# Kernel optimization log

Measured on AMD Instinct MI355X. Metric: run time of the kernel, lower is better.

The kernel has to match this reference:

```python
import jax, jax.numpy as jnp
import numpy as np

N_QUBITS = 12
N_LAYERS = 3
N_PARAMS = N_QUBITS * 3 * N_LAYERS  # 108
BATCH = 8192
DIM = 1 << N_QUBITS  # 4096


def _rx(theta):
    c = jnp.cos(theta / 2).astype(jnp.complex64)
    s = jnp.sin(theta / 2).astype(jnp.complex64)
    return jnp.stack([jnp.stack([c, -1j * s]), jnp.stack([-1j * s, c])])


def _ry(theta):
    c = jnp.cos(theta / 2).astype(jnp.complex64)
    s = jnp.sin(theta / 2).astype(jnp.complex64)
    return jnp.stack([jnp.stack([c, -s]), jnp.stack([s, c])])


def _rz(theta):
    e = jnp.exp(-1j * theta.astype(jnp.complex64) / 2)
    z = jnp.zeros((), jnp.complex64)
    return jnp.stack([jnp.stack([e, z]), jnp.stack([z, jnp.conj(e)])])


def _apply_1q(state, q, U):
    # state: (B,) + (2,)*n ; apply 2x2 gate U on wire q (axis q+1)
    s = jnp.moveaxis(state, q + 1, -1)
    s = s @ U.T
    return jnp.moveaxis(s, -1, q + 1)


def _cnot(state, c, t):
    # control wire c, target wire t (axes offset by 1 for batch dim)
    ca, ta = c + 1, t + 1
    s0 = jax.lax.index_in_dim(state, 0, ca, keepdims=False)
    s1 = jax.lax.index_in_dim(state, 1, ca, keepdims=False)
    ta2 = ta - 1 if ta > ca else ta  # target axis shifts after removing control axis
    s1 = jnp.flip(s1, axis=ta2)  # X on target (size-2 axis)
    return jnp.stack([s0, s1], axis=ca)


def setup_inputs() -> dict:
    key = jax.random.key(0)
    k1, k2 = jax.random.split(key)
    x = jax.random.normal(k1, (BATCH, DIM), dtype=jnp.float32)
    params = jax.random.normal(k2, (N_PARAMS,), dtype=jnp.float32) * 0.1
    return {"x": x, "params": params}


def reference(x, params):
    n = N_QUBITS
    B = x.shape[0]
    # AmplitudeEmbedding with normalize=True
    norm = jnp.linalg.norm(x, axis=1, keepdims=True)
    state = (x / norm).astype(jnp.complex64).reshape((B,) + (2,) * n)
    idx = 0
    for _ in range(N_LAYERS):
        for q in range(n):
            state = _apply_1q(state, q, _rx(params[idx])); idx += 1
            state = _apply_1q(state, q, _ry(params[idx])); idx += 1
            state = _apply_1q(state, q, _rz(params[idx])); idx += 1
        for q in range(n):
            state = _cnot(state, q, (q + 1) % n)
    # <Z_q> = P(q=0) - P(q=1)
    p = state.real ** 2 + state.imag ** 2  # (B,) + (2,)*n, float32
    outs = []
    for q in range(n):
        axes = tuple(a for a in range(1, n + 1) if a != q + 1)
        marg = jnp.sum(p, axis=axes)  # (B, 2)
        outs.append(marg[:, 0] - marg[:, 1])
    return jnp.stack(outs, axis=1)  # (B, n_qubits)
```

## Files before the change

kernel.cpp:

```cpp
#include <hip/hip_runtime.h>
#include <math.h>

#define NQ 12
#define DIM 4096
#define NGATES 36
#define NROUND 9

typedef float f32x2 __attribute__((ext_vector_type(2)));

constexpr unsigned swz(unsigned x) { return x ^ (x >> 4); }

struct Round {
  unsigned s[4];
  unsigned l[4];
  unsigned cbsw8[16];
};
struct PlanT {
  Round rd[NROUND];
  unsigned zsel[NQ];
};

constexpr PlanT make_plan() {
  PlanT P{};
  unsigned Mcol[NQ] = {}, Minv[NQ] = {};
  for (int i = 0; i < NQ; ++i) { Mcol[i] = 1u << i; Minv[i] = 1u << i; }
  unsigned gm[NGATES] = {}, gs[NGATES] = {};
  int g = 0;
  for (int L = 0; L < 3; ++L) {
    for (int q = 0; q < NQ; ++q) { int b = NQ - 1 - q; gm[g] = Mcol[b]; gs[g] = Minv[b]; ++g; }
    for (int q = 0; q < NQ; ++q) {
      int bc = NQ - 1 - q, bt = NQ - 1 - ((q + 1) % NQ);
      Mcol[bc] ^= Mcol[bt];
      Minv[bt] ^= Minv[bc];
    }
  }
  for (int r = 0; r < NROUND; ++r) {
    unsigned m[4], red[4];
    for (int k = 0; k < 4; ++k) { m[k] = gm[4*r+k]; red[k] = m[k]; P.rd[r].s[k] = gs[4*r+k]; }
    for (int a = 0; a < 4; ++a) {
      unsigned p = red[a] & (0u - red[a]);
      for (int b = a + 1; b < 4; ++b) if (red[b] & p) red[b] ^= red[a];
    }
    unsigned piv[4];
    for (int a = 0; a < 4; ++a) piv[a] = red[a] & (0u - red[a]);
    for (int a = 0; a < 4; ++a)
      for (int b = a + 1; b < 4; ++b)
        if (piv[a] > piv[b]) { unsigned tp = piv[a]; piv[a] = piv[b]; piv[b] = tp; }
    for (int a = 0; a < 4; ++a) P.rd[r].l[a] = piv[a] - 1u;
    for (int d = 0; d < 16; ++d) {
      unsigned c = 0;
      for (int k = 0; k < 4; ++k) if (d & (1 << k)) c ^= m[k];
      P.rd[r].cbsw8[d] = swz(c) << 3;
    }
  }
  for (int q = 0; q < NQ; ++q) P.zsel[q] = Minv[NQ - 1 - q];
  return P;
}

constexpr PlanT PLAN = make_plan();

__global__ void qc_prep(const float* __restrict__ params, f32x2* __restrict__ gpk) {
  int t = threadIdx.x;
  if (t < NGATES) {
    float h1 = params[3*t+0]*0.5f, h2 = params[3*t+1]*0.5f, h3 = params[3*t+2]*0.5f;
    float c1 = cosf(h1), s1 = sinf(h1);
    float c2 = cosf(h2), s2 = sinf(h2);
    float c3 = cosf(h3), s3 = sinf(h3);
    float a00r =  c2*c1, a00i =  s2*s1;
    float a01r = -s2*c1, a01i = -c2*s1;
    float a10r =  s2*c1, a10i = -c2*s1;
    float a11r =  c2*c1, a11i = -s2*s1;
    float u[8];
    u[0] = c3*a00r + s3*a00i;  u[1] = c3*a00i - s3*a00r;
    u[2] = c3*a01r + s3*a01i;  u[3] = c3*a01i - s3*a01r;
    u[4] = c3*a10r - s3*a10i;  u[5] = c3*a10i + s3*a10r;
    u[6] = c3*a11r - s3*a11i;  u[7] = c3*a11i + s3*a11r;
    f32x2* o = gpk + t*8;
#pragma unroll
    for (int k = 0; k < 4; ++k) {
      f32x2 a, b;
      a[0] =  u[2*k];   a[1] = u[2*k+1];
      b[0] = -u[2*k+1]; b[1] = u[2*k];
      o[2*k]   = a;
      o[2*k+1] = b;
    }
  }
}

__device__ __forceinline__ f32x2 blo(f32x2 a) { return __builtin_shufflevector(a, a, 0, 0); }
__device__ __forceinline__ f32x2 bhi(f32x2 a) { return __builtin_shufflevector(a, a, 1, 1); }

__global__ __launch_bounds__(256)
__attribute__((amdgpu_waves_per_eu(5, 5)))
void qc_main(const float* __restrict__ x, const f32x2* __restrict__ gpk,
             float* __restrict__ out) {
  __shared__ float2 sst[DIM];
  char* sb = (char*)sst;
  float* sf = (float*)sst;
  const int t = threadIdx.x;
  const long row = blockIdx.x;

  const float4* x4 = (const float4*)(x + (size_t)row * DIM);
  float ssq = 0.f;
#pragma unroll
  for (int k = 0; k < 4; ++k) {
    float4 a = x4[t + 256*k];
    int j0 = 4*(t + 256*k);
    *(float2*)(sb + (swz((unsigned)j0)     << 3)) = make_float2(a.x, 0.f);
    *(float2*)(sb + (swz((unsigned)(j0+1)) << 3)) = make_float2(a.y, 0.f);
    *(float2*)(sb + (swz((unsigned)(j0+2)) << 3)) = make_float2(a.z, 0.f);
    *(float2*)(sb + (swz((unsigned)(j0+3)) << 3)) = make_float2(a.w, 0.f);
    ssq += a.x*a.x + a.y*a.y + a.z*a.z + a.w*a.w;
  }
#pragma unroll
  for (int off = 32; off > 0; off >>= 1) ssq += __shfl_down(ssq, off, 64);
  __syncthreads();

#pragma unroll 1
  for (int r = 0; r < NROUND; ++r) {
    const unsigned s0 = PLAN.rd[r].s[0], sA = PLAN.rd[r].s[1];
    const unsigned sB = PLAN.rd[r].s[2], sC = PLAN.rd[r].s[3];
    const unsigned l0 = PLAN.rd[r].l[0], l1 = PLAN.rd[r].l[1];
    const unsigned l2 = PLAN.rd[r].l[2], l3 = PLAN.rd[r].l[3];
    unsigned cb[16];
#pragma unroll
    for (int d = 0; d < 16; ++d) cb[d] = PLAN.rd[r].cbsw8[d];

    unsigned j = (unsigned)t;
    j = ((j & ~l0) << 1) | (j & l0);
    j = ((j & ~l1) << 1) | (j & l1);
    j = ((j & ~l2) << 1) | (j & l2);
    j = ((j & ~l3) << 1) | (j & l3);
    unsigned adj8 = 0;
    adj8 ^= (unsigned)(-(int)(__popc(j & s0) & 1)) & cb[1];
    adj8 ^= (unsigned)(-(int)(__popc(j & sA) & 1)) & cb[2];
    adj8 ^= (unsigned)(-(int)(__popc(j & sB) & 1)) & cb[4];
    adj8 ^= (unsigned)(-(int)(__popc(j & sC) & 1)) & cb[8];
    const unsigned base8 = ((j ^ (j >> 4)) << 3) ^ adj8;

    f32x2 v[16];
#pragma unroll
    for (int d = 0; d < 16; ++d)
      v[d] = *(const f32x2*)(sb + (base8 ^ cb[d]));

#pragma unroll
    for (int st = 0; st < 4; ++st) {
      const f32x2* cp = gpk + (r * 4 + st) * 8;
      const f32x2 c0 = cp[0], c1 = cp[1], c2 = cp[2], c3 = cp[3];
      const f32x2 c4 = cp[4], c5 = cp[5], c6 = cp[6], c7 = cp[7];
#pragma unroll
      for (int d = 0; d < 16; ++d) {
        if (!(d & (1 << st))) {
          const int d1 = d | (1 << st);
          const f32x2 a0 = v[d], a1 = v[d1];
          f32x2 o0 = c0 * blo(a0);
          o0 += c1 * bhi(a0);
          o0 += c2 * blo(a1);
          o0 += c3 * bhi(a1);
          f32x2 o1 = c4 * blo(a0);
          o1 += c5 * bhi(a0);
          o1 += c6 * blo(a1);
          o1 += c7 * bhi(a1);
          v[d] = o0; v[d1] = o1;
        }
      }
    }
#pragma unroll
    for (int d = 0; d < 16; ++d)
      *(f32x2*)(sb + (base8 ^ cb[d])) = v[d];
    __syncthreads();
  }

  const unsigned mbase8 = (((16u * (unsigned)t) ^ (unsigned)t) << 3);
  float p[16];
#pragma unroll
  for (int c = 0; c < 16; ++c) {
    f32x2 v = *(const f32x2*)(sb + (mbase8 ^ ((unsigned)c << 3)));
    f32x2 sq = v * v;
    p[c] = sq[0] + sq[1];
  }
#pragma unroll
  for (int b = 0; b < 4; ++b) {
#pragma unroll
    for (int c = 0; c < 16; ++c) {
      if (!(c & (1 << b))) {
        const int c1 = c | (1 << b);
        float u = p[c], v = p[c1];
        p[c] = u + v; p[c1] = u - v;
      }
    }
  }
  float zs[NQ];
#pragma unroll
  for (int q = 0; q < NQ; ++q) {
    const unsigned m = PLAN.zsel[q];
    const float v = p[m & 15u];
    const int sgn = __popc((unsigned)t & (m >> 4)) & 1;
    zs[q] = sgn ? -v : v;
  }
#pragma unroll
  for (int q = 0; q < NQ; ++q) {
#pragma unroll
    for (int off = 32; off > 0; off >>= 1) zs[q] += __shfl_down(zs[q], off, 64);
  }
  __syncthreads();
  const int w = t >> 6;
  if ((t & 63) == 0) {
#pragma unroll
    for (int q = 0; q < NQ; ++q) sf[w*NQ + q] = zs[q];
    sf[48 + w] = ssq;
  }
  __syncthreads();
  if (t < NQ) {
    const float den = sf[48] + sf[49] + sf[50] + sf[51];
    const float tot = sf[t] + sf[NQ + t] + sf[2*NQ + t] + sf[3*NQ + t];
    out[row * NQ + t] = tot / den;
  }
}

extern "C" void kernel_launch(void* const* d_in, const int* in_sizes, int n_in,
                              void* d_out, int out_size, void* d_ws, size_t ws_size,
                              hipStream_t stream) {
  const float* x = (const float*)d_in[0];
  const float* params = (const float*)d_in[1];
  float* out = (float*)d_out;
  f32x2* gpk = (f32x2*)d_ws;
  const int nrows = in_sizes[0] / DIM;
  qc_prep<<<dim3(1), dim3(64), 0, stream>>>(params, gpk);
  qc_main<<<dim3(nrows), dim3(256), 0, stream>>>(x, gpk, out);
}
```

Measured before the change: 358.4 us.

## Fuse three gates per round with 512 threads instead of four with 256

Changes the gate-fusion granularity from 4 gates per shared-memory round (16 amplitudes per thread, 256 threads) to 3 gates per round (8 amplitudes per thread, 512 threads), which gives 12 rounds instead of 9. Each thread holds half as many registers, so occupancy can rise (waves_per_eu 8). The cost is more shared-memory passes and barriers per row. The marginal reduction and the final cross-wave sum are adjusted for 8 waves.

```diff
diff --git a/kernel.cpp b/kernel.cpp
--- a/kernel.cpp
+++ b/kernel.cpp
@@ -4,16 +4,19 @@
 #define NQ 12
 #define DIM 4096
 #define NGATES 36
-#define NROUND 9
+#define NB 3
+#define NSLOT 8
+#define NROUND 12
+#define THREADS 512
 
 typedef float f32x2 __attribute__((ext_vector_type(2)));
 
 constexpr unsigned swz(unsigned x) { return x ^ (x >> 4); }
 
 struct Round {
-  unsigned s[4];
-  unsigned l[4];
-  unsigned cbsw8[16];
+  unsigned s[NB];
+  unsigned l[NB];
+  unsigned cbsw8[NSLOT];
 };
 struct PlanT {
   Round rd[NROUND];
@@ -35,21 +38,21 @@
     }
   }
   for (int r = 0; r < NROUND; ++r) {
-    unsigned m[4], red[4];
-    for (int k = 0; k < 4; ++k) { m[k] = gm[4*r+k]; red[k] = m[k]; P.rd[r].s[k] = gs[4*r+k]; }
-    for (int a = 0; a < 4; ++a) {
+    unsigned m[NB], red[NB];
+    for (int k = 0; k < NB; ++k) { m[k] = gm[NB*r+k]; red[k] = m[k]; P.rd[r].s[k] = gs[NB*r+k]; }
+    for (int a = 0; a < NB; ++a) {
       unsigned p = red[a] & (0u - red[a]);
-      for (int b = a + 1; b < 4; ++b) if (red[b] & p) red[b] ^= red[a];
-    }
-    unsigned piv[4];
-    for (int a = 0; a < 4; ++a) piv[a] = red[a] & (0u - red[a]);
-    for (int a = 0; a < 4; ++a)
-      for (int b = a + 1; b < 4; ++b)
+      for (int b = a + 1; b < NB; ++b) if (red[b] & p) red[b] ^= red[a];
+    }
+    unsigned piv[NB];
+    for (int a = 0; a < NB; ++a) piv[a] = red[a] & (0u - red[a]);
+    for (int a = 0; a < NB; ++a)
+      for (int b = a + 1; b < NB; ++b)
         if (piv[a] > piv[b]) { unsigned tp = piv[a]; piv[a] = piv[b]; piv[b] = tp; }
-    for (int a = 0; a < 4; ++a) P.rd[r].l[a] = piv[a] - 1u;
-    for (int d = 0; d < 16; ++d) {
+    for (int a = 0; a < NB; ++a) P.rd[r].l[a] = piv[a] - 1u;
+    for (int d = 0; d < NSLOT; ++d) {
       unsigned c = 0;
-      for (int k = 0; k < 4; ++k) if (d & (1 << k)) c ^= m[k];
+      for (int k = 0; k < NB; ++k) if (d & (1 << k)) c ^= m[k];
       P.rd[r].cbsw8[d] = swz(c) << 3;
     }
   }
@@ -90,8 +93,8 @@
 __device__ __forceinline__ f32x2 blo(f32x2 a) { return __builtin_shufflevector(a, a, 0, 0); }
 __device__ __forceinline__ f32x2 bhi(f32x2 a) { return __builtin_shufflevector(a, a, 1, 1); }
 
-__global__ __launch_bounds__(256)
-__attribute__((amdgpu_waves_per_eu(5, 5)))
+__global__ __launch_bounds__(THREADS)
+__attribute__((amdgpu_waves_per_eu(8, 8)))
 void qc_main(const float* __restrict__ x, const f32x2* __restrict__ gpk,
              float* __restrict__ out) {
   __shared__ float2 sst[DIM];
@@ -103,9 +106,9 @@
   const float4* x4 = (const float4*)(x + (size_t)row * DIM);
   float ssq = 0.f;
 #pragma unroll
-  for (int k = 0; k < 4; ++k) {
-    float4 a = x4[t + 256*k];
-    int j0 = 4*(t + 256*k);
+  for (int k = 0; k < 2; ++k) {
+    float4 a = x4[t + THREADS*k];
+    int j0 = 4*(t + THREADS*k);
     *(float2*)(sb + (swz((unsigned)j0)     << 3)) = make_float2(a.x, 0.f);
     *(float2*)(sb + (swz((unsigned)(j0+1)) << 3)) = make_float2(a.y, 0.f);
     *(float2*)(sb + (swz((unsigned)(j0+2)) << 3)) = make_float2(a.z, 0.f);
@@ -118,38 +121,34 @@
 
 #pragma unroll 1
   for (int r = 0; r < NROUND; ++r) {
-    const unsigned s0 = PLAN.rd[r].s[0], sA = PLAN.rd[r].s[1];
-    const unsigned sB = PLAN.rd[r].s[2], sC = PLAN.rd[r].s[3];
-    const unsigned l0 = PLAN.rd[r].l[0], l1 = PLAN.rd[r].l[1];
-    const unsigned l2 = PLAN.rd[r].l[2], l3 = PLAN.rd[r].l[3];
-    unsigned cb[16];
-#pragma unroll
-    for (int d = 0; d < 16; ++d) cb[d] = PLAN.rd[r].cbsw8[d];
+    const unsigned s0 = PLAN.rd[r].s[0], sA = PLAN.rd[r].s[1], sB = PLAN.rd[r].s[2];
+    const unsigned l0 = PLAN.rd[r].l[0], l1 = PLAN.rd[r].l[1], l2 = PLAN.rd[r].l[2];
+    unsigned cb[NSLOT];
+#pragma unroll
+    for (int d = 0; d < NSLOT; ++d) cb[d] = PLAN.rd[r].cbsw8[d];
 
     unsigned j = (unsigned)t;
     j = ((j & ~l0) << 1) | (j & l0);
     j = ((j & ~l1) << 1) | (j & l1);
     j = ((j & ~l2) << 1) | (j & l2);
-    j = ((j & ~l3) << 1) | (j & l3);
     unsigned adj8 = 0;
     adj8 ^= (unsigned)(-(int)(__popc(j & s0) & 1)) & cb[1];
     adj8 ^= (unsigned)(-(int)(__popc(j & sA) & 1)) & cb[2];
     adj8 ^= (unsigned)(-(int)(__popc(j & sB) & 1)) & cb[4];
-    adj8 ^= (unsigned)(-(int)(__popc(j & sC) & 1)) & cb[8];
     const unsigned base8 = ((j ^ (j >> 4)) << 3) ^ adj8;
 
-    f32x2 v[16];
-#pragma unroll
-    for (int d = 0; d < 16; ++d)
+    f32x2 v[NSLOT];
+#pragma unroll
+    for (int d = 0; d < NSLOT; ++d)
       v[d] = *(const f32x2*)(sb + (base8 ^ cb[d]));
 
 #pragma unroll
-    for (int st = 0; st < 4; ++st) {
-      const f32x2* cp = gpk + (r * 4 + st) * 8;
+    for (int st = 0; st < NB; ++st) {
+      const f32x2* cp = gpk + (r * NB + st) * 8;
       const f32x2 c0 = cp[0], c1 = cp[1], c2 = cp[2], c3 = cp[3];
       const f32x2 c4 = cp[4], c5 = cp[5], c6 = cp[6], c7 = cp[7];
 #pragma unroll
-      for (int d = 0; d < 16; ++d) {
+      for (int d = 0; d < NSLOT; ++d) {
         if (!(d & (1 << st))) {
           const int d1 = d | (1 << st);
           const f32x2 a0 = v[d], a1 = v[d1];
@@ -166,23 +165,23 @@
       }
     }
 #pragma unroll
-    for (int d = 0; d < 16; ++d)
+    for (int d = 0; d < NSLOT; ++d)
       *(f32x2*)(sb + (base8 ^ cb[d])) = v[d];
     __syncthreads();
   }
 
-  const unsigned mbase8 = (((16u * (unsigned)t) ^ (unsigned)t) << 3);
-  float p[16];
-#pragma unroll
-  for (int c = 0; c < 16; ++c) {
+  const unsigned mbase8 = (((8u * (unsigned)t) ^ ((unsigned)t >> 1)) << 3);
+  float p[NSLOT];
+#pragma unroll
+  for (int c = 0; c < NSLOT; ++c) {
     f32x2 v = *(const f32x2*)(sb + (mbase8 ^ ((unsigned)c << 3)));
     f32x2 sq = v * v;
     p[c] = sq[0] + sq[1];
   }
 #pragma unroll
-  for (int b = 0; b < 4; ++b) {
-#pragma unroll
-    for (int c = 0; c < 16; ++c) {
+  for (int b = 0; b < NB; ++b) {
+#pragma unroll
+    for (int c = 0; c < NSLOT; ++c) {
       if (!(c & (1 << b))) {
         const int c1 = c | (1 << b);
         float u = p[c], v = p[c1];
@@ -194,8 +193,8 @@
 #pragma unroll
   for (int q = 0; q < NQ; ++q) {
     const unsigned m = PLAN.zsel[q];
-    const float v = p[m & 15u];
-    const int sgn = __popc((unsigned)t & (m >> 4)) & 1;
+    const float v = p[m & 7u];
+    const int sgn = __popc((unsigned)t & (m >> 3)) & 1;
     zs[q] = sgn ? -v : v;
   }
 #pragma unroll
@@ -208,12 +207,13 @@
   if ((t & 63) == 0) {
 #pragma unroll
     for (int q = 0; q < NQ; ++q) sf[w*NQ + q] = zs[q];
-    sf[48 + w] = ssq;
+    sf[96 + w] = ssq;
   }
   __syncthreads();
   if (t < NQ) {
-    const float den = sf[48] + sf[49] + sf[50] + sf[51];
-    const float tot = sf[t] + sf[NQ + t] + sf[2*NQ + t] + sf[3*NQ + t];
+    float den = 0.f, tot = 0.f;
+#pragma unroll
+    for (int k = 0; k < 8; ++k) { den += sf[96 + k]; tot += sf[k*NQ + t]; }
     out[row * NQ + t] = tot / den;
   }
 }
@@ -227,5 +227,5 @@
   f32x2* gpk = (f32x2*)d_ws;
   const int nrows = in_sizes[0] / DIM;
   qc_prep<<<dim3(1), dim3(64), 0, stream>>>(params, gpk);
-  qc_main<<<dim3(nrows), dim3(256), 0, stream>>>(x, gpk, out);
-}
+  qc_main<<<dim3(nrows), dim3(THREADS), 0, stream>>>(x, gpk, out);
+}
```

Measured after the change: 375.6 us. +4.8%, slower.

## Apply fused 4-qubit gate rounds via split-fp16 MFMA matrix multiplies

Applied to the files above, without the earlier changes.

Each round's four single-qubit gates are combined into a 16x16 complex matrix, built as a Kronecker product in the prep kernel. The matrix is stored as hi/lo fp16 splits in a real-embedded layout, and the state is also split into hi/lo fp16 so that 16x16x32 f16 MFMA instructions can apply the round. This replaces the scalar packed-FMA butterfly per gate, and the occupancy hint is relaxed. It trades VALU work for matrix-core work plus extra conversion ops. Precision now relies on a two-term fp16 split, and the hi-lo-lo cross term is included.

```diff
diff --git a/kernel.cpp b/kernel.cpp
--- a/kernel.cpp
+++ b/kernel.cpp
@@ -6,7 +6,10 @@
 #define NGATES 36
 #define NROUND 9
 
-typedef float f32x2 __attribute__((ext_vector_type(2)));
+typedef float f32x4 __attribute__((ext_vector_type(4)));
+typedef __fp16 fp16x2 __attribute__((ext_vector_type(2)));
+typedef __fp16 fp16x4 __attribute__((ext_vector_type(4)));
+typedef __fp16 fp16x8 __attribute__((ext_vector_type(8)));
 
 constexpr unsigned swz(unsigned x) { return x ^ (x >> 4); }
 
@@ -14,6 +17,7 @@
   unsigned s[4];
   unsigned l[4];
   unsigned cbsw8[16];
+  unsigned dt[4];
 };
 struct PlanT {
   Round rd[NROUND];
@@ -52,6 +56,18 @@
       for (int k = 0; k < 4; ++k) if (d & (1 << k)) c ^= m[k];
       P.rd[r].cbsw8[d] = swz(c) << 3;
     }
+    for (int tt = 0; tt < 4; ++tt) {
+      unsigned c = (unsigned)tt << 4;
+      unsigned j = c;
+      j = ((j & ~P.rd[r].l[0]) << 1) | (j & P.rd[r].l[0]);
+      j = ((j & ~P.rd[r].l[1]) << 1) | (j & P.rd[r].l[1]);
+      j = ((j & ~P.rd[r].l[2]) << 1) | (j & P.rd[r].l[2]);
+      j = ((j & ~P.rd[r].l[3]) << 1) | (j & P.rd[r].l[3]);
+      unsigned d = swz(j) << 3;
+      for (int k = 0; k < 4; ++k)
+        if (__builtin_popcount(j & P.rd[r].s[k]) & 1) d ^= P.rd[r].cbsw8[1u << k];
+      P.rd[r].dt[tt] = d;
+    }
   }
   for (int q = 0; q < NQ; ++q) P.zsel[q] = Minv[NQ - 1 - q];
   return P;
@@ -59,40 +75,53 @@
 
 constexpr PlanT PLAN = make_plan();
 
-__global__ void qc_prep(const float* __restrict__ params, f32x2* __restrict__ gpk) {
+__global__ void qc_prep(const float* __restrict__ params, __fp16* __restrict__ amat) {
   int t = threadIdx.x;
-  if (t < NGATES) {
-    float h1 = params[3*t+0]*0.5f, h2 = params[3*t+1]*0.5f, h3 = params[3*t+2]*0.5f;
+  int r = t >> 4, s = t & 15;
+  if (r >= NROUND) return;
+  float U[4][8];
+  for (int k = 0; k < 4; ++k) {
+    int gg = r * 4 + k;
+    float h1 = params[3*gg+0]*0.5f, hh2 = params[3*gg+1]*0.5f, h3 = params[3*gg+2]*0.5f;
     float c1 = cosf(h1), s1 = sinf(h1);
-    float c2 = cosf(h2), s2 = sinf(h2);
+    float c2 = cosf(hh2), s2 = sinf(hh2);
     float c3 = cosf(h3), s3 = sinf(h3);
     float a00r =  c2*c1, a00i =  s2*s1;
     float a01r = -s2*c1, a01i = -c2*s1;
     float a10r =  s2*c1, a10i = -c2*s1;
     float a11r =  c2*c1, a11i = -s2*s1;
-    float u[8];
-    u[0] = c3*a00r + s3*a00i;  u[1] = c3*a00i - s3*a00r;
-    u[2] = c3*a01r + s3*a01i;  u[3] = c3*a01i - s3*a01r;
-    u[4] = c3*a10r - s3*a10i;  u[5] = c3*a10i + s3*a10r;
-    u[6] = c3*a11r - s3*a11i;  u[7] = c3*a11i + s3*a11r;
-    f32x2* o = gpk + t*8;
-#pragma unroll
+    U[k][0] = c3*a00r + s3*a00i;  U[k][1] = c3*a00i - s3*a00r;
+    U[k][2] = c3*a01r + s3*a01i;  U[k][3] = c3*a01i - s3*a01r;
+    U[k][4] = c3*a10r - s3*a10i;  U[k][5] = c3*a10i + s3*a10r;
+    U[k][6] = c3*a11r - s3*a11i;  U[k][7] = c3*a11i + s3*a11r;
+  }
+  __fp16* b0 = amat + r*2048 + s*32;
+  __fp16* b1 = b0 + 512;
+  __fp16* b2 = b0 + 1024;
+  __fp16* b3 = b0 + 1536;
+  for (int j = 0; j < 16; ++j) {
+    float pr = 1.f, pi = 0.f;
     for (int k = 0; k < 4; ++k) {
-      f32x2 a, b;
-      a[0] =  u[2*k];   a[1] = u[2*k+1];
-      b[0] = -u[2*k+1]; b[1] = u[2*k];
-      o[2*k]   = a;
-      o[2*k+1] = b;
-    }
-  }
-}
-
-__device__ __forceinline__ f32x2 blo(f32x2 a) { return __builtin_shufflevector(a, a, 0, 0); }
-__device__ __forceinline__ f32x2 bhi(f32x2 a) { return __builtin_shufflevector(a, a, 1, 1); }
+      int idx = ((((s >> k) & 1) * 2) + ((j >> k) & 1)) * 2;
+      float gr = U[k][idx], gi = U[k][idx + 1];
+      float npr = pr * gr - pi * gi;
+      pi = pr * gi + pi * gr;
+      pr = npr;
+    }
+    float v0_ =  pr; __fp16 e0 = (__fp16)v0_;
+    float v1_ = -pi; __fp16 e1 = (__fp16)v1_;
+    float v2_ =  pi; __fp16 e2 = (__fp16)v2_;
+    float v3_ =  pr; __fp16 e3 = (__fp16)v3_;
+    b0[2*j]   = e0;  b1[2*j]   = (__fp16)(v0_ - (float)e0);
+    b0[2*j+1] = e1;  b1[2*j+1] = (__fp16)(v1_ - (float)e1);
+    b2[2*j]   = e2;  b3[2*j]   = (__fp16)(v2_ - (float)e2);
+    b2[2*j+1] = e3;  b3[2*j+1] = (__fp16)(v3_ - (float)e3);
+  }
+}
 
 __global__ __launch_bounds__(256)
-__attribute__((amdgpu_waves_per_eu(5, 5)))
-void qc_main(const float* __restrict__ x, const f32x2* __restrict__ gpk,
+__attribute__((amdgpu_waves_per_eu(4, 5)))
+void qc_main(const float* __restrict__ x, const __fp16* __restrict__ amat,
              float* __restrict__ out) {
   __shared__ float2 sst[DIM];
   char* sb = (char*)sst;
@@ -122,52 +151,71 @@
     const unsigned sB = PLAN.rd[r].s[2], sC = PLAN.rd[r].s[3];
     const unsigned l0 = PLAN.rd[r].l[0], l1 = PLAN.rd[r].l[1];
     const unsigned l2 = PLAN.rd[r].l[2], l3 = PLAN.rd[r].l[3];
-    unsigned cb[16];
-#pragma unroll
-    for (int d = 0; d < 16; ++d) cb[d] = PLAN.rd[r].cbsw8[d];
-
-    unsigned j = (unsigned)t;
+    const unsigned CB1 = PLAN.rd[r].cbsw8[1], CB2 = PLAN.rd[r].cbsw8[2];
+    const unsigned CB3 = PLAN.rd[r].cbsw8[3];
+    const unsigned C4 = PLAN.rd[r].cbsw8[4], C8 = PLAN.rd[r].cbsw8[8];
+    const unsigned D1 = PLAN.rd[r].dt[1], D2 = PLAN.rd[r].dt[2];
+    const unsigned D3 = PLAN.rd[r].dt[3];
+
+    unsigned j = ((unsigned)t & 0xC0u) | ((unsigned)t & 15u);
     j = ((j & ~l0) << 1) | (j & l0);
     j = ((j & ~l1) << 1) | (j & l1);
     j = ((j & ~l2) << 1) | (j & l2);
     j = ((j & ~l3) << 1) | (j & l3);
     unsigned adj8 = 0;
-    adj8 ^= (unsigned)(-(int)(__popc(j & s0) & 1)) & cb[1];
-    adj8 ^= (unsigned)(-(int)(__popc(j & sA) & 1)) & cb[2];
-    adj8 ^= (unsigned)(-(int)(__popc(j & sB) & 1)) & cb[4];
-    adj8 ^= (unsigned)(-(int)(__popc(j & sC) & 1)) & cb[8];
-    const unsigned base8 = ((j ^ (j >> 4)) << 3) ^ adj8;
-
-    f32x2 v[16];
-#pragma unroll
-    for (int d = 0; d < 16; ++d)
-      v[d] = *(const f32x2*)(sb + (base8 ^ cb[d]));
-
-#pragma unroll
-    for (int st = 0; st < 4; ++st) {
-      const f32x2* cp = gpk + (r * 4 + st) * 8;
-      const f32x2 c0 = cp[0], c1 = cp[1], c2 = cp[2], c3 = cp[3];
-      const f32x2 c4 = cp[4], c5 = cp[5], c6 = cp[6], c7 = cp[7];
-#pragma unroll
-      for (int d = 0; d < 16; ++d) {
-        if (!(d & (1 << st))) {
-          const int d1 = d | (1 << st);
-          const f32x2 a0 = v[d], a1 = v[d1];
-          f32x2 o0 = c0 * blo(a0);
-          o0 += c1 * bhi(a0);
-          o0 += c2 * blo(a1);
-          o0 += c3 * bhi(a1);
-          f32x2 o1 = c4 * blo(a0);
-          o1 += c5 * bhi(a0);
-          o1 += c6 * blo(a1);
-          o1 += c7 * bhi(a1);
-          v[d] = o0; v[d1] = o1;
-        }
-      }
-    }
-#pragma unroll
-    for (int d = 0; d < 16; ++d)
-      *(f32x2*)(sb + (base8 ^ cb[d])) = v[d];
+    adj8 ^= (unsigned)(-(int)(__popc(j & s0) & 1)) & CB1;
+    adj8 ^= (unsigned)(-(int)(__popc(j & sA) & 1)) & CB2;
+    adj8 ^= (unsigned)(-(int)(__popc(j & sB) & 1)) & C4;
+    adj8 ^= (unsigned)(-(int)(__popc(j & sC) & 1)) & C8;
+    const unsigned q = ((unsigned)t >> 4) & 3u;
+    const unsigned qsel = ((q & 1u) ? C4 : 0u) ^ ((q & 2u) ? C8 : 0u);
+    const unsigned b0a = (((j ^ (j >> 4)) << 3) ^ adj8) ^ qsel;
+
+    const fp16x8* am = (const fp16x8*)(amat + (size_t)r * 2048);
+    const int fo = (t & 15) * 4 + (int)q;
+    const fp16x8 Arh = am[fo];
+    const fp16x8 Arl = am[64 + fo];
+    const fp16x8 Aih = am[128 + fo];
+    const fp16x8 Ail = am[192 + fo];
+
+#pragma unroll
+    for (int tt = 0; tt < 4; ++tt) {
+      const unsigned bb = b0a ^ (tt == 0 ? 0u : tt == 1 ? D1 : tt == 2 ? D2 : D3);
+      const unsigned a0 = bb, a1 = bb ^ CB1, a2 = bb ^ CB2, a3 = bb ^ CB3;
+      const float2 A0 = *(const float2*)(sb + a0);
+      const float2 A1 = *(const float2*)(sb + a1);
+      const float2 A2 = *(const float2*)(sb + a2);
+      const float2 A3 = *(const float2*)(sb + a3);
+      fp16x2 p0 = __builtin_amdgcn_cvt_pkrtz(A0.x, A0.y);
+      fp16x2 p1 = __builtin_amdgcn_cvt_pkrtz(A1.x, A1.y);
+      fp16x2 p2 = __builtin_amdgcn_cvt_pkrtz(A2.x, A2.y);
+      fp16x2 p3 = __builtin_amdgcn_cvt_pkrtz(A3.x, A3.y);
+      fp16x2 q0 = __builtin_amdgcn_cvt_pkrtz(A0.x - (float)p0[0], A0.y - (float)p0[1]);
+      fp16x2 q1 = __builtin_amdgcn_cvt_pkrtz(A1.x - (float)p1[0], A1.y - (float)p1[1]);
+      fp16x2 q2 = __builtin_amdgcn_cvt_pkrtz(A2.x - (float)p2[0], A2.y - (float)p2[1]);
+      fp16x2 q3 = __builtin_amdgcn_cvt_pkrtz(A3.x - (float)p3[0], A3.y - (float)p3[1]);
+      fp16x4 u01 = __builtin_shufflevector(p0, p1, 0, 1, 2, 3);
+      fp16x4 u23 = __builtin_shufflevector(p2, p3, 0, 1, 2, 3);
+      fp16x8 Bhi = __builtin_shufflevector(u01, u23, 0, 1, 2, 3, 4, 5, 6, 7);
+      fp16x4 w01 = __builtin_shufflevector(q0, q1, 0, 1, 2, 3);
+      fp16x4 w23 = __builtin_shufflevector(q2, q3, 0, 1, 2, 3);
+      fp16x8 Blo = __builtin_shufflevector(w01, w23, 0, 1, 2, 3, 4, 5, 6, 7);
+
+      f32x4 are = {0.f, 0.f, 0.f, 0.f}, aim = {0.f, 0.f, 0.f, 0.f};
+      are = __builtin_amdgcn_mfma_f32_16x16x32_f16(Arh, Bhi, are, 0, 0, 0);
+      are = __builtin_amdgcn_mfma_f32_16x16x32_f16(Arl, Bhi, are, 0, 0, 0);
+      are = __builtin_amdgcn_mfma_f32_16x16x32_f16(Arh, Blo, are, 0, 0, 0);
+      are = __builtin_amdgcn_mfma_f32_16x16x32_f16(Arl, Blo, are, 0, 0, 0);
+      aim = __builtin_amdgcn_mfma_f32_16x16x32_f16(Aih, Bhi, aim, 0, 0, 0);
+      aim = __builtin_amdgcn_mfma_f32_16x16x32_f16(Ail, Bhi, aim, 0, 0, 0);
+      aim = __builtin_amdgcn_mfma_f32_16x16x32_f16(Aih, Blo, aim, 0, 0, 0);
+      aim = __builtin_amdgcn_mfma_f32_16x16x32_f16(Ail, Blo, aim, 0, 0, 0);
+
+      *(float2*)(sb + a0) = make_float2(are[0], aim[0]);
+      *(float2*)(sb + a1) = make_float2(are[1], aim[1]);
+      *(float2*)(sb + a2) = make_float2(are[2], aim[2]);
+      *(float2*)(sb + a3) = make_float2(are[3], aim[3]);
+    }
     __syncthreads();
   }
 
@@ -175,9 +223,8 @@
   float p[16];
 #pragma unroll
   for (int c = 0; c < 16; ++c) {
-    f32x2 v = *(const f32x2*)(sb + (mbase8 ^ ((unsigned)c << 3)));
-    f32x2 sq = v * v;
-    p[c] = sq[0] + sq[1];
+    float2 v = *(const float2*)(sb + (mbase8 ^ ((unsigned)c << 3)));
+    p[c] = v.x * v.x + v.y * v.y;
   }
 #pragma unroll
   for (int b = 0; b < 4; ++b) {
@@ -192,22 +239,22 @@
   }
   float zs[NQ];
 #pragma unroll
-  for (int q = 0; q < NQ; ++q) {
-    const unsigned m = PLAN.zsel[q];
+  for (int qq = 0; qq < NQ; ++qq) {
+    const unsigned m = PLAN.zsel[qq];
     const float v = p[m & 15u];
     const int sgn = __popc((unsigned)t & (m >> 4)) & 1;
-    zs[q] = sgn ? -v : v;
-  }
-#pragma unroll
-  for (int q = 0; q < NQ; ++q) {
-#pragma unroll
-    for (int off = 32; off > 0; off >>= 1) zs[q] += __shfl_down(zs[q], off, 64);
+    zs[qq] = sgn ? -v : v;
+  }
+#pragma unroll
+  for (int qq = 0; qq < NQ; ++qq) {
+#pragma unroll
+    for (int off = 32; off > 0; off >>= 1) zs[qq] += __shfl_down(zs[qq], off, 64);
   }
   __syncthreads();
   const int w = t >> 6;
   if ((t & 63) == 0) {
 #pragma unroll
-    for (int q = 0; q < NQ; ++q) sf[w*NQ + q] = zs[q];
+    for (int qq = 0; qq < NQ; ++qq) sf[w*NQ + qq] = zs[qq];
     sf[48 + w] = ssq;
   }
   __syncthreads();
@@ -224,8 +271,8 @@
   const float* x = (const float*)d_in[0];
   const float* params = (const float*)d_in[1];
   float* out = (float*)d_out;
-  f32x2* gpk = (f32x2*)d_ws;
+  __fp16* amat = (__fp16*)d_ws;
   const int nrows = in_sizes[0] / DIM;
-  qc_prep<<<dim3(1), dim3(64), 0, stream>>>(params, gpk);
-  qc_main<<<dim3(nrows), dim3(256), 0, stream>>>(x, gpk, out);
-}
+  qc_prep<<<dim3(1), dim3(256), 0, stream>>>(params, amat);
+  qc_main<<<dim3(nrows), dim3(256), 0, stream>>>(x, amat, out);
+}
```

After: 327.2 us. 1.1x faster.
